# Kernel tuning notes

Hardware: AMD Instinct MI355X
Metric: run time of the kernel (lower is better)

## Reference

```python
import jax, jax.numpy as jnp
import numpy as np

N, D = 8192, 256
NUM_CLASSES = 64


def setup_inputs() -> dict:
    key = jax.random.key(0)
    k1, k2 = jax.random.split(key)
    represent = jax.random.normal(k1, (N, D), dtype=jnp.float32)
    label = jax.random.randint(k2, (N,), 0, NUM_CLASSES, dtype=jnp.int64)
    t = jnp.float32(0.1)  # temperature
    return {"represent": represent, "label": label, "t": t}


def reference(represent, label, t):
    x = represent.astype(jnp.float32)                      # [N, D]
    norms = jnp.sqrt(jnp.sum(x * x, axis=-1))              # [N]
    # pairwise cosine: (x x^T) / (||xi|| ||xj||)
    cos = (x @ x.T) / (norms[:, None] * norms[None, :])    # [N, N]
    pos_mask = label[:, None] == label[None, :]            # [N, N] bool
    e = jnp.exp(cos / t)                                   # [N, N]
    # original computes exp(mask * cos / t): masked-out entries become exp(0) = 1
    pos_pair = jnp.where(pos_mask, e, 1.0).sum(axis=-1)    # [N]
    neg_pair = jnp.where(pos_mask, 1.0, e).sum(axis=-1)    # [N]
    loss = (jnp.log(neg_pair) - jnp.log(pos_pair)).sum() / represent.shape[0]
    return loss
```

## Files before the change

### kernel.cpp

```cpp
#include <hip/hip_runtime.h>

#define N_ROWS 8192
#define DIM 256
#define NUM_CLASSES 64
#define NBLK 64
#define NTRI (NBLK * (NBLK + 1) / 2)
#define SCR_PITCH 36

typedef float f32x4 __attribute__((ext_vector_type(4)));

__device__ __forceinline__ void gload_lds16(const void* g, void* l) {
  __builtin_amdgcn_global_load_lds(
      (const __attribute__((address_space(1))) unsigned int*)g,
      (__attribute__((address_space(3))) unsigned int*)l, 16, 0, 0);
}

__device__ __forceinline__ void tri_decode(int q, int& I, int& J) {
  int i = (int)((129.0f - sqrtf(16641.0f - 8.0f * (float)q)) * 0.5f);
  while (i * (129 - i) / 2 > q) --i;
  while ((i + 1) * (128 - i) / 2 <= q) ++i;
  I = i;
  J = i + (q - i * (129 - i) / 2);
}

__global__ void __launch_bounds__(256) prep_kernel(
    const float* __restrict__ x, const int* __restrict__ lab,
    const float* __restrict__ tptr, unsigned int* __restrict__ xq,
    float* __restrict__ sv, int* __restrict__ hpart,
    float* __restrict__ gsum, unsigned int* __restrict__ gcnt) {
  const int tid = threadIdx.x;
  if (blockIdx.x == 0 && tid == 0) { *gsum = 0.f; *gcnt = 0u; }
  const int row = blockIdx.x * 4 + (tid >> 6);
  const int lane = tid & 63;
  const float4 v = *reinterpret_cast<const float4*>(x + (size_t)row * DIM + lane * 4);
  int p = __builtin_amdgcn_cvt_pk_fp8_f32(v.x, v.y, 0, false);
  p = __builtin_amdgcn_cvt_pk_fp8_f32(v.z, v.w, p, true);
  const float f0 = __builtin_amdgcn_cvt_f32_fp8(p, 0);
  const float f1 = __builtin_amdgcn_cvt_f32_fp8(p, 1);
  const float f2 = __builtin_amdgcn_cvt_f32_fp8(p, 2);
  const float f3 = __builtin_amdgcn_cvt_f32_fp8(p, 3);
  float ss = f0 * f0 + f1 * f1 + f2 * f2 + f3 * f3;
  xq[(size_t)row * 64 + lane] = (unsigned int)p;
  for (int m = 32; m; m >>= 1) ss += __shfl_xor(ss, m, 64);
  if (lane == 0) sv[row] = sqrtf(1.4426950408889634f / tptr[0] / ss);

  if (blockIdx.x < 32) {
    __shared__ int h[NUM_CLASSES];
    if (tid < NUM_CLASSES) h[tid] = 0;
    __syncthreads();
    atomicAdd(&h[lab[blockIdx.x * 256 + tid]], 1);
    __syncthreads();
    if (tid < NUM_CLASSES) hpart[blockIdx.x * NUM_CLASSES + tid] = h[tid];
  }
}

__global__ void __launch_bounds__(256, 3) main_kernel(
    const unsigned char* __restrict__ xb, const float* __restrict__ sv,
    const int* __restrict__ lab, float2* __restrict__ part) {
  const int q = blockIdx.x;
  int I, J;
  tri_decode(q, I, J);
  const int rowBase = I * 128;
  const int colBase = J * 128;

  __shared__ alignas(16) unsigned char buf[36864];
  __shared__ float colred[2][128][2];
  __shared__ float rsv[128]; __shared__ int rlab[128];
  __shared__ float csv[128]; __shared__ int clab[128];
  unsigned char* Al = buf;
  unsigned char* Bl = buf + 16384;
  float* scr0 = reinterpret_cast<float*>(buf);
  float* scr1 = reinterpret_cast<float*>(buf + 18432);

  const int tid = threadIdx.x;
  const int wave = tid >> 6;
  const int lane = tid & 63;
  const int quad = lane >> 4;
  const int lc = lane & 15;
  const int wrow = (wave >> 1) * 64;
  const int wcol = (wave & 1) * 64;
  const int ch = wave & 1;
  const int r8 = lane >> 3;
  const int c8 = lane & 7;

  if (tid < 128) {
    rsv[tid] = sv[rowBase + tid];
    rlab[tid] = lab[rowBase + tid];
    csv[tid] = sv[colBase + tid];
    clab[tid] = lab[colBase + tid];
  }

  const unsigned char* Ag = xb + (size_t)rowBase * DIM;
  const unsigned char* Bg = xb + (size_t)colBase * DIM;

#define STAGE_HALF(h)                                                         \
  {                                                                           \
    _Pragma("unroll") for (int i = 0; i < 4; ++i) {                           \
      const int r = wave * 32 + i * 8 + r8;                                   \
      const int gc = c8 ^ (r & 7);                                            \
      gload_lds16(Ag + (size_t)r * 256 + (h)*128 + gc * 16,                   \
                  Al + (wave * 32 + i * 8) * 128);                            \
      gload_lds16(Bg + (size_t)r * 256 + (h)*128 + gc * 16,                   \
                  Bl + (wave * 32 + i * 8) * 128);                            \
    }                                                                         \
  }

  f32x4 acc[4][4];
  const f32x4 zero4 = {0.f, 0.f, 0.f, 0.f};
  for (int mi = 0; mi < 4; ++mi)
    for (int ni = 0; ni < 4; ++ni) acc[mi][ni] = zero4;

  const int qh = quad >> 1, h8 = (quad & 1) * 8;
  int aOff[4], bOff[4];
#pragma unroll
  for (int mi = 0; mi < 4; ++mi)
    aOff[mi] = (wrow + mi * 16 + lc) * 128 + h8;
#pragma unroll
  for (int ni = 0; ni < 4; ++ni)
    bOff[ni] = (wcol + ni * 16 + lc) * 128 + h8;

  STAGE_HALF(0)
  __syncthreads();
#pragma unroll
  for (int half = 0; half < 2; ++half) {
#pragma unroll
    for (int kbl = 0; kbl < 4; ++kbl) {
      const int swz = (((kbl * 2 + qh) ^ (lc & 7)) << 4);
      long afr[4], bfr[4];
#pragma unroll
      for (int mi = 0; mi < 4; ++mi)
        afr[mi] = *reinterpret_cast<const long*>(Al + aOff[mi] + swz);
#pragma unroll
      for (int ni = 0; ni < 4; ++ni)
        bfr[ni] = *reinterpret_cast<const long*>(Bl + bOff[ni] + swz);
#pragma unroll
      for (int mi = 0; mi < 4; ++mi)
#pragma unroll
        for (int ni = 0; ni < 4; ++ni)
          acc[mi][ni] = __builtin_amdgcn_mfma_f32_16x16x32_fp8_fp8(
              afr[mi], bfr[ni], acc[mi][ni], 0, 0, 0);
    }
    __syncthreads();
    if (half == 0) {
      STAGE_HALF(1)
      __syncthreads();
    }
  }
#undef STAGE_HALF

  float scol[4];
  int labc[4];
#pragma unroll
  for (int ni = 0; ni < 4; ++ni) {
    scol[ni] = csv[wcol + ni * 16 + lc];
    labc[ni] = clab[wcol + ni * 16 + lc];
  }
  float ctot[4] = {0.f, 0.f, 0.f, 0.f};
  float csame[4] = {0.f, 0.f, 0.f, 0.f};

#pragma unroll
  for (int mi = 0; mi < 4; ++mi) {
#pragma unroll
    for (int r = 0; r < 4; ++r) {
      const int lr = wrow + mi * 16 + quad * 4 + r;
      const float siv = rsv[lr];
      const int li = rlab[lr];
      float st = 0.f, sm = 0.f;
#pragma unroll
      for (int ni = 0; ni < 4; ++ni) {
        const float e = exp2f(acc[mi][ni][r] * (siv * scol[ni]));
        const float em = (li == labc[ni]) ? e : 0.f;
        st += e;
        sm += em;
        ctot[ni] += e;
        csame[ni] += em;
      }
      scr0[lr * SCR_PITCH + ch * 16 + lc] = st;
      scr1[lr * SCR_PITCH + ch * 16 + lc] = sm;
    }
  }

  if (J > I) {
#pragma unroll
    for (int ni = 0; ni < 4; ++ni) {
      float t2 = ctot[ni] + __shfl_xor(ctot[ni], 16, 64);
      t2 += __shfl_xor(t2, 32, 64);
      float s2 = csame[ni] + __shfl_xor(csame[ni], 16, 64);
      s2 += __shfl_xor(s2, 32, 64);
      if (quad == 0) {
        colred[0][wcol + ni * 16 + lc][wave >> 1] = t2;
        colred[1][wcol + ni * 16 + lc][wave >> 1] = s2;
      }
    }
  }
  __syncthreads();

  if (tid < 128) {
    const int base = tid * SCR_PITCH;
    f32x4 a0 = {0.f, 0.f, 0.f, 0.f}, a1 = {0.f, 0.f, 0.f, 0.f};
#pragma unroll
    for (int k = 0; k < 8; ++k)
      a0 += *reinterpret_cast<const f32x4*>(&scr0[base + 4 * k]);
#pragma unroll
    for (int k = 0; k < 8; ++k)
      a1 += *reinterpret_cast<const f32x4*>(&scr1[base + 4 * k]);
    float2 v;
    v.x = a0[0] + a0[1] + a0[2] + a0[3];
    v.y = a1[0] + a1[1] + a1[2] + a1[3];
    part[(size_t)J * N_ROWS + rowBase + tid] = v;
    if (J > I) {
      float2 w;
      w.x = colred[0][tid][0] + colred[0][tid][1];
      w.y = colred[1][tid][0] + colred[1][tid][1];
      part[(size_t)I * N_ROWS + colBase + tid] = w;
    }
  }
}

__global__ void __launch_bounds__(256) row_loss_kernel(
    const float2* __restrict__ part, const int* __restrict__ lab,
    const int* __restrict__ hpart, float* __restrict__ gsum,
    unsigned int* __restrict__ gcnt, float* __restrict__ out) {
  __shared__ int h[NUM_CLASSES];
  if (threadIdx.x < NUM_CLASSES) {
    int s = 0;
#pragma unroll
    for (int k = 0; k < 32; ++k) s += hpart[k * NUM_CLASSES + threadIdx.x];
    h[threadIdx.x] = s;
  }
  __syncthreads();

  const int row = blockIdx.x * 256 + threadIdx.x;
  float st = 0.f, sm = 0.f;
#pragma unroll 8
  for (int b = 0; b < 64; ++b) {
    const float2 v = part[(size_t)b * N_ROWS + row];
    st += v.x;
    sm += v.y;
  }
  const int c = h[lab[row]];
  const float pos = sm + (float)(N_ROWS - c);
  const float neg = (st - sm) + (float)c;
  float term = logf(neg) - logf(pos);
  for (int m = 32; m; m >>= 1) term += __shfl_xor(term, m, 64);
  __shared__ float wsum[4];
  const int lane = threadIdx.x & 63;
  const int wave = threadIdx.x >> 6;
  if (lane == 0) wsum[wave] = term;
  __syncthreads();
  if (threadIdx.x == 0) {
    atomicAdd(gsum, wsum[0] + wsum[1] + wsum[2] + wsum[3]);
    __threadfence();
    const unsigned int t = atomicAdd(gcnt, 1u);
    if (t == (unsigned int)(N_ROWS / 256 - 1)) {
      const float total = atomicAdd(gsum, 0.0f);
      out[0] = total * (1.0f / (float)N_ROWS);
    }
  }
}

extern "C" void kernel_launch(void* const* d_in, const int* in_sizes, int n_in,
                              void* d_out, int out_size, void* d_ws, size_t ws_size,
                              hipStream_t stream) {
  const float* x = (const float*)d_in[0];
  const int* lab = (const int*)d_in[1];
  const float* t = (const float*)d_in[2];
  float* out = (float*)d_out;

  char* ws = (char*)d_ws;
  unsigned int* xq = (unsigned int*)ws;
  float* sv = (float*)(ws + (2u << 20));
  float2* part = (float2*)(ws + (2u << 20) + (32u << 10));
  float* gsum = (float*)(ws + (6u << 20) + (32u << 10));
  unsigned int* gcnt = (unsigned int*)(ws + (6u << 20) + (32u << 10) + 8);
  int* hpart = (int*)(ws + (6u << 20) + (33u << 10));

  prep_kernel<<<N_ROWS / 4, 256, 0, stream>>>(x, lab, t, xq, sv, hpart, gsum, gcnt);
  main_kernel<<<NTRI, 256, 0, stream>>>((const unsigned char*)xq, sv, lab, part);
  row_loss_kernel<<<N_ROWS / 256, 256, 0, stream>>>(part, lab, hpart, gsum, gcnt, out);
}
```

Measured before the change: 96.54 us.

## Prefetch second K-half into registers and interleave row-sum scratch as float2

```diff
diff --git a/kernel.cpp b/kernel.cpp
--- a/kernel.cpp
+++ b/kernel.cpp
@@ -5,7 +5,7 @@
 #define NUM_CLASSES 64
 #define NBLK 64
 #define NTRI (NBLK * (NBLK + 1) / 2)
-#define SCR_PITCH 36
+#define SCR_PITCH2 34
 
 typedef float f32x4 __attribute__((ext_vector_type(4)));
 
@@ -63,14 +63,13 @@
   const int rowBase = I * 128;
   const int colBase = J * 128;
 
-  __shared__ alignas(16) unsigned char buf[36864];
+  __shared__ alignas(16) unsigned char buf[34816];
   __shared__ float colred[2][128][2];
   __shared__ float rsv[128]; __shared__ int rlab[128];
   __shared__ float csv[128]; __shared__ int clab[128];
   unsigned char* Al = buf;
   unsigned char* Bl = buf + 16384;
-  float* scr0 = reinterpret_cast<float*>(buf);
-  float* scr1 = reinterpret_cast<float*>(buf + 18432);
+  float2* scr = reinterpret_cast<float2*>(buf);
 
   const int tid = threadIdx.x;
   const int wave = tid >> 6;
@@ -93,16 +92,20 @@
   const unsigned char* Ag = xb + (size_t)rowBase * DIM;
   const unsigned char* Bg = xb + (size_t)colBase * DIM;
 
-#define STAGE_HALF(h)                                                         \
-  {                                                                           \
-    _Pragma("unroll") for (int i = 0; i < 4; ++i) {                           \
-      const int r = wave * 32 + i * 8 + r8;                                   \
-      const int gc = c8 ^ (r & 7);                                            \
-      gload_lds16(Ag + (size_t)r * 256 + (h)*128 + gc * 16,                   \
-                  Al + (wave * 32 + i * 8) * 128);                            \
-      gload_lds16(Bg + (size_t)r * 256 + (h)*128 + gc * 16,                   \
-                  Bl + (wave * 32 + i * 8) * 128);                            \
-    }                                                                         \
+  float4 pfa[4], pfb[4];
+#pragma unroll
+  for (int i = 0; i < 4; ++i) {
+    const int r = wave * 32 + i * 8 + r8;
+    const int gc = c8 ^ (r & 7);
+    gload_lds16(Ag + (size_t)r * 256 + gc * 16, Al + (wave * 32 + i * 8) * 128);
+    gload_lds16(Bg + (size_t)r * 256 + gc * 16, Bl + (wave * 32 + i * 8) * 128);
+  }
+#pragma unroll
+  for (int i = 0; i < 4; ++i) {
+    const int r = wave * 32 + i * 8 + r8;
+    const int gc = c8 ^ (r & 7);
+    pfa[i] = *reinterpret_cast<const float4*>(Ag + (size_t)r * 256 + 128 + gc * 16);
+    pfb[i] = *reinterpret_cast<const float4*>(Bg + (size_t)r * 256 + 128 + gc * 16);
   }
 
   f32x4 acc[4][4];
@@ -119,8 +122,8 @@
   for (int ni = 0; ni < 4; ++ni)
     bOff[ni] = (wcol + ni * 16 + lc) * 128 + h8;
 
-  STAGE_HALF(0)
-  __syncthreads();
+  __syncthreads();
+
 #pragma unroll
   for (int half = 0; half < 2; ++half) {
 #pragma unroll
@@ -142,11 +145,15 @@
     }
     __syncthreads();
     if (half == 0) {
-      STAGE_HALF(1)
+#pragma unroll
+      for (int i = 0; i < 4; ++i) {
+        const int dst = (wave * 32 + i * 8 + r8) * 128 + c8 * 16;
+        *reinterpret_cast<float4*>(Al + dst) = pfa[i];
+        *reinterpret_cast<float4*>(Bl + dst) = pfb[i];
+      }
       __syncthreads();
     }
   }
-#undef STAGE_HALF
 
   float scol[4];
   int labc[4];
@@ -175,8 +182,8 @@
         ctot[ni] += e;
         csame[ni] += em;
       }
-      scr0[lr * SCR_PITCH + ch * 16 + lc] = st;
-      scr1[lr * SCR_PITCH + ch * 16 + lc] = sm;
+      float2 w; w.x = st; w.y = sm;
+      scr[lr * SCR_PITCH2 + ch * 16 + lc] = w;
     }
   }
 
@@ -196,17 +203,17 @@
   __syncthreads();
 
   if (tid < 128) {
-    const int base = tid * SCR_PITCH;
-    f32x4 a0 = {0.f, 0.f, 0.f, 0.f}, a1 = {0.f, 0.f, 0.f, 0.f};
-#pragma unroll
-    for (int k = 0; k < 8; ++k)
-      a0 += *reinterpret_cast<const f32x4*>(&scr0[base + 4 * k]);
-#pragma unroll
-    for (int k = 0; k < 8; ++k)
-      a1 += *reinterpret_cast<const f32x4*>(&scr1[base + 4 * k]);
-    float2 v;
-    v.x = a0[0] + a0[1] + a0[2] + a0[3];
-    v.y = a1[0] + a1[1] + a1[2] + a1[3];
+    const float2* row = scr + tid * SCR_PITCH2;
+    const int rot = tid >> 3;
+    float st = 0.f, sm = 0.f;
+#pragma unroll
+    for (int k = 0; k < 16; ++k) {
+      const int kk = ((k + rot) & 15) * 2;
+      const f32x4 c = *reinterpret_cast<const f32x4*>(row + kk);
+      st += c[0] + c[2];
+      sm += c[1] + c[3];
+    }
+    float2 v; v.x = st; v.y = sm;
     part[(size_t)J * N_ROWS + rowBase + tid] = v;
     if (J > I) {
       float2 w;
```

Result: slower. 104.6 us (+8.3%).
